# Kernel optimization log

Hardware: AMD Instinct MI355X
Metric: run time of the kernel (lower is better)

The kernel has to match this reference:

```python
import jax, jax.numpy as jnp
import numpy as np

NEG_BIG = -9e15  # matches torch's -9000000000000000.0 mask value
LRELU_ALPHA = 0.2


def setup_inputs() -> dict:
    key = jax.random.key(0)
    ks = jax.random.split(key, 6)
    B, N, Fin, Fout = 2, 4096, 64, 64
    x = jax.random.normal(ks[0], (B, N, Fin), jnp.float32)
    pos = jax.random.normal(ks[1], (B, N, 3), jnp.float32)
    # xavier-ish scaled params
    W = jax.random.normal(ks[2], (Fin, Fout), jnp.float32) * (1.0 / np.sqrt(Fin))
    a = jax.random.normal(ks[3], (2 * Fout, 1), jnp.float32) * (1.0 / np.sqrt(2 * Fout))
    Wp = jax.random.normal(ks[4], (3, Fout), jnp.float32) * (1.0 / np.sqrt(3))
    bp = jnp.zeros((Fout,), jnp.float32)
    return {"x": x, "pos": pos, "W": W, "a": a, "Wp": Wp, "bp": bp, "k": 20}


def reference(x, pos, W, a, Wp, bp, k):
    B, N, _ = x.shape
    Fout = W.shape[1]
    Wh = x @ W  # [B,N,Fout]

    # Dynamic kNN graph (adj=None path): squared-distance ranking == cdist ranking
    sq = jnp.sum(pos * pos, axis=-1)  # [B,N]
    d2 = sq[:, :, None] + sq[:, None, :] - 2.0 * jnp.einsum('bnd,bmd->bnm', pos, pos)
    _, idx = jax.lax.top_k(-d2, k + 1)  # smallest k+1 distances
    idx = idx[:, :, 1:]  # drop self
    adj = jnp.zeros((B, N, N), x.dtype).at[
        jnp.arange(B)[:, None, None], jnp.arange(N)[None, :, None], idx
    ].set(1.0)

    # e[b,i,j] = leakyrelu(a1.Wh_i + a2.Wh_j); decompose instead of O(N^2*2F) concat
    f1 = Wh @ a[:Fout]  # [B,N,1]
    f2 = Wh @ a[Fout:]  # [B,N,1]
    e = f1 + jnp.swapaxes(f2, 1, 2)  # [B,N,N]
    e = jnp.where(e > 0, e, LRELU_ALPHA * e)

    e = jnp.where(adj > 0, e, NEG_BIG)
    attn = jax.nn.softmax(e, axis=2)  # dropout is identity in eval mode

    h = jnp.einsum('bnm,bmf->bnf', attn, Wh) + jax.nn.relu(pos @ Wp + bp)
    return jax.nn.elu(h)  # concat=True path
```

## Files before the change

kernel.cpp:

```cpp
#include <hip/hip_runtime.h>
#include <cfloat>

#define NB 4096
#define FD 64
#define EPT 16
#define QPB 4
#define LRELU_ALPHA 0.2f
#define CCAP 128

__global__ void wa_kernel(const float* __restrict__ W, const float* __restrict__ a,
                          float* __restrict__ wa) {
    const int t = threadIdx.x;
    const float* av = a + ((t >> 6) << 6);
    const int i = t & 63;
    float s = 0.f;
    #pragma unroll
    for (int j = 0; j < FD; ++j) s = fmaf(W[i * FD + j], av[j], s);
    wa[t] = s;
}

__global__ __launch_bounds__(256) void gat_fused(
    const float* __restrict__ x, const float* __restrict__ pos,
    const float* __restrict__ W, const float* __restrict__ wa,
    const float* __restrict__ Wp, const float* __restrict__ bp,
    const int* __restrict__ kptr, float* __restrict__ out)
{
    __shared__ unsigned long long upool[QPB * CCAP];
    __shared__ float4 sq[QPB];
    __shared__ float sT[QPB];
    __shared__ unsigned int cnt[QPB];
    __shared__ int idx21[QPB][64];

    float* tmin = (float*)upool;
    unsigned long long (*cand)[CCAP] = (unsigned long long(*)[CCAP])upool;

    const int tid = threadIdx.x;
    const int lane = tid & 63, wave = tid >> 6;
    const int qbase = blockIdx.x * QPB;
    const int b = qbase >> 12;
    const float* posb = pos + (size_t)b * NB * 3;
    const int k = *kptr;

    if (tid < QPB) {
        const int nq = (qbase + tid) & (NB - 1);
        const float ax = posb[nq * 3 + 0], ay = posb[nq * 3 + 1], az = posb[nq * 3 + 2];
        const float sr = __fadd_rn(__fadd_rn(__fmul_rn(ax, ax), __fmul_rn(ay, ay)),
                                   __fmul_rn(az, az));
        sq[tid] = make_float4(ax, ay, az, sr);
        cnt[tid] = 0;
    }
    __syncthreads();

    const float4 q0 = sq[0], q1 = sq[1], q2 = sq[2], q3 = sq[3];

    const float4* p4 = (const float4*)posb;
    float f0 = FLT_MAX, f1m = FLT_MAX, f2m = FLT_MAX, f3m = FLT_MAX;
    #pragma unroll
    for (int c = 0; c < 4; ++c) {
        const float4 a0 = p4[tid * 12 + c * 3 + 0];
        const float4 a1 = p4[tid * 12 + c * 3 + 1];
        const float4 a2 = p4[tid * 12 + c * 3 + 2];
        const float pxs[4] = {a0.x, a0.w, a1.z, a2.y};
        const float pys[4] = {a0.y, a1.x, a1.w, a2.z};
        const float pzs[4] = {a0.z, a1.y, a2.x, a2.w};
        #pragma unroll
        for (int j = 0; j < 4; ++j) {
            const float px = pxs[j], py = pys[j], pz = pzs[j];
            const float sm = fmaf(pz, pz, fmaf(py, py, px * px));
            float d;
            d = fmaf(-2.f, fmaf(q0.x, px, fmaf(q0.y, py, q0.z * pz)), q0.w + sm);
            f0 = fminf(f0, d);
            d = fmaf(-2.f, fmaf(q1.x, px, fmaf(q1.y, py, q1.z * pz)), q1.w + sm);
            f1m = fminf(f1m, d);
            d = fmaf(-2.f, fmaf(q2.x, px, fmaf(q2.y, py, q2.z * pz)), q2.w + sm);
            f2m = fminf(f2m, d);
            d = fmaf(-2.f, fmaf(q3.x, px, fmaf(q3.y, py, q3.z * pz)), q3.w + sm);
            f3m = fminf(f3m, d);
        }
    }
    tmin[0 * 256 + tid] = f0;  tmin[1 * 256 + tid] = f1m;
    tmin[2 * 256 + tid] = f2m; tmin[3 * 256 + tid] = f3m;
    __syncthreads();

    float v = fminf(fminf(tmin[wave * 256 + lane],       tmin[wave * 256 + 64 + lane]),
                    fminf(tmin[wave * 256 + 128 + lane], tmin[wave * 256 + 192 + lane]));
    #pragma unroll
    for (int kk2 = 2; kk2 <= 64; kk2 <<= 1) {
        #pragma unroll
        for (int j = kk2 >> 1; j > 0; j >>= 1) {
            const float o = __shfl_xor(v, j, 64);
            const bool keepMin = (((lane & j) == 0) == ((lane & kk2) == 0));
            v = keepMin ? fminf(v, o) : fmaxf(v, o);
        }
    }
    const float Tq = __shfl(v, k, 64);
    if (lane == 0) sT[wave] = Tq;
    __syncthreads();

    const float Ts0 = sT[0] + 1e-2f + 1e-3f * fabsf(sT[0]);
    const float Ts1 = sT[1] + 1e-2f + 1e-3f * fabsf(sT[1]);
    const float Ts2 = sT[2] + 1e-2f + 1e-3f * fabsf(sT[2]);
    const float Ts3 = sT[3] + 1e-2f + 1e-3f * fabsf(sT[3]);

    #pragma unroll
    for (int c = 0; c < 4; ++c) {
        const float4 a0 = p4[tid * 12 + c * 3 + 0];
        const float4 a1 = p4[tid * 12 + c * 3 + 1];
        const float4 a2 = p4[tid * 12 + c * 3 + 2];
        const float pxs[4] = {a0.x, a0.w, a1.z, a2.y};
        const float pys[4] = {a0.y, a1.x, a1.w, a2.z};
        const float pzs[4] = {a0.z, a1.y, a2.x, a2.w};
        #pragma unroll
        for (int j = 0; j < 4; ++j) {
            const float px = pxs[j], py = pys[j], pz = pzs[j];
            const float sm = fmaf(pz, pz, fmaf(py, py, px * px));
            const int m = tid * EPT + c * 4 + j;
            #pragma unroll
            for (int q = 0; q < QPB; ++q) {
                const float4 qq = (q == 0) ? q0 : (q == 1) ? q1 : (q == 2) ? q2 : q3;
                const float Tsl = (q == 0) ? Ts0 : (q == 1) ? Ts1 : (q == 2) ? Ts2 : Ts3;
                const float d = fmaf(-2.f, fmaf(qq.x, px, fmaf(qq.y, py, qq.z * pz)),
                                     qq.w + sm);
                if (d <= Tsl) {
                    const float sqm = __fadd_rn(__fadd_rn(__fmul_rn(px, px),
                                                          __fmul_rn(py, py)),
                                                __fmul_rn(pz, pz));
                    const float dot = __fadd_rn(__fadd_rn(__fmul_rn(qq.x, px),
                                                          __fmul_rn(qq.y, py)),
                                                __fmul_rn(qq.z, pz));
                    const float d2 = __fsub_rn(__fadd_rn(qq.w, sqm),
                                               __fmul_rn(2.0f, dot));
                    const unsigned int u = __float_as_uint(d2);
                    const unsigned int kk = u ^ ((unsigned int)((int)u >> 31) | 0x80000000u);
                    const unsigned long long pk =
                        ((unsigned long long)kk << 12) | (unsigned int)m;
                    const unsigned int p = atomicAdd(&cnt[q], 1u);
                    if (p < CCAP) cand[q][p] = pk;
                }
            }
        }
    }
    __syncthreads();

    const int cn0 = (int)cnt[wave];
    const int cn = cn0 < CCAP ? cn0 : CCAP;
    for (int e = lane; e < cn; e += 64) {
        const unsigned long long xv = cand[wave][e];
        int r = 0;
        for (int j = 0; j < cn; ++j) r += (cand[wave][j] < xv);
        if (r <= k) idx21[wave][r] = (int)(xv & 0xFFFu);
    }

    const int row = qbase + wave;
    const int nself = row & (NB - 1);
    const float4 qq = sq[wave];
    const float* xb = x + (((size_t)b << 12) << 6);
    const float wa1v = wa[lane], wa2v = wa[FD + lane];

    float p1 = xb[((size_t)nself << 6) + lane] * wa1v;
    #pragma unroll
    for (int off = 32; off > 0; off >>= 1) p1 += __shfl_xor(p1, off, 64);
    const float f1v = p1;

    float esc = 0.f;
    for (int t = 1; t <= k; ++t) {
        const int nb_ = idx21[wave][t];
        float pm = xb[((size_t)nb_ << 6) + lane] * wa2v;
        #pragma unroll
        for (int off = 32; off > 0; off >>= 1) pm += __shfl_xor(pm, off, 64);
        if (lane == t) esc = pm;
    }
    const bool valid = (lane >= 1 && lane <= k);
    float e = valid ? f1v + esc : -FLT_MAX;
    if (valid) e = e > 0.f ? e : LRELU_ALPHA * e;
    float mx = e;
    #pragma unroll
    for (int off = 32; off > 0; off >>= 1) mx = fmaxf(mx, __shfl_xor(mx, off, 64));
    const float ex = valid ? __expf(e - mx) : 0.f;
    float Z = ex;
    #pragma unroll
    for (int off = 32; off > 0; off >>= 1) Z += __shfl_xor(Z, off, 64);
    const float attn = ex / Z;

    float g = 0.f;
    for (int t = 1; t <= k; ++t) {
        const int nb_ = idx21[wave][t];
        const float xr = xb[((size_t)nb_ << 6) + lane];
        g = fmaf(__shfl(attn, t, 64), xr, g);
    }

    float h = 0.f;
    #pragma unroll 8
    for (int kk = 0; kk < FD; ++kk)
        h = fmaf(__shfl(g, kk, 64), W[kk * FD + lane], h);

    const float pv = fmaf(qq.x, Wp[0 * FD + lane],
                     fmaf(qq.y, Wp[1 * FD + lane],
                     fmaf(qq.z, Wp[2 * FD + lane], bp[lane])));
    h += pv > 0.f ? pv : 0.f;
    out[((size_t)row << 6) + lane] = h > 0.f ? h : expm1f(h);
}

extern "C" void kernel_launch(void* const* d_in, const int* in_sizes, int n_in,
                              void* d_out, int out_size, void* d_ws, size_t ws_size,
                              hipStream_t stream) {
    const float* x   = (const float*)d_in[0];
    const float* pos = (const float*)d_in[1];
    const float* W   = (const float*)d_in[2];
    const float* a   = (const float*)d_in[3];
    const float* Wp  = (const float*)d_in[4];
    const float* bp  = (const float*)d_in[5];
    const int*   kp  = (const int*)d_in[6];
    float* wa  = (float*)d_ws;
    float* out = (float*)d_out;

    wa_kernel<<<1, 128, 0, stream>>>(W, a, wa);
    gat_fused<<<(NB * 2) / QPB, 256, 0, stream>>>(x, pos, W, wa, Wp, bp, kp, out);
}
```

Measured before the change: 111.7 us.

## Precompute Wh and attention logits in prep kernel; defer exact distance to candidates

```diff
diff --git a/kernel.cpp b/kernel.cpp
--- a/kernel.cpp
+++ b/kernel.cpp
@@ -3,36 +3,59 @@
 
 #define NB 4096
 #define FD 64
-#define EPT 16
 #define QPB 4
 #define LRELU_ALPHA 0.2f
-#define CCAP 128
-
-__global__ void wa_kernel(const float* __restrict__ W, const float* __restrict__ a,
-                          float* __restrict__ wa) {
-    const int t = threadIdx.x;
-    const float* av = a + ((t >> 6) << 6);
-    const int i = t & 63;
-    float s = 0.f;
-    #pragma unroll
-    for (int j = 0; j < FD; ++j) s = fmaf(W[i * FD + j], av[j], s);
-    wa[t] = s;
+#define CCAP 96
+
+__global__ __launch_bounds__(256) void prep_kernel(
+    const float* __restrict__ x, const float* __restrict__ W,
+    const float* __restrict__ a,
+    float* __restrict__ Wh, float* __restrict__ f1, float* __restrict__ f2)
+{
+    __shared__ float sW[FD * FD];
+    const int tid = threadIdx.x;
+    #pragma unroll
+    for (int t = 0; t < 16; ++t) sW[tid + t * 256] = W[tid + t * 256];
+    __syncthreads();
+    const int lane = tid & 63, wave = tid >> 6;
+    const float a1v = a[lane], a2v = a[FD + lane];
+    const int rbase = blockIdx.x * 32 + wave * 8;
+    #pragma unroll 2
+    for (int j = 0; j < 8; ++j) {
+        const int row = rbase + j;
+        const float xv = x[((size_t)row << 6) + lane];
+        float acc = 0.f;
+        #pragma unroll
+        for (int i = 0; i < FD; ++i)
+            acc = fmaf(__shfl(xv, i, 64), sW[i * FD + lane], acc);
+        Wh[((size_t)row << 6) + lane] = acc;
+        float r1 = acc * a1v, r2 = acc * a2v;
+        #pragma unroll
+        for (int off = 32; off > 0; off >>= 1) {
+            r1 += __shfl_down(r1, off, 64);
+            r2 += __shfl_down(r2, off, 64);
+        }
+        if (lane == 0) { f1[row] = r1; f2[row] = r2; }
+    }
 }
 
 __global__ __launch_bounds__(256) void gat_fused(
-    const float* __restrict__ x, const float* __restrict__ pos,
-    const float* __restrict__ W, const float* __restrict__ wa,
+    const float* __restrict__ pos, const float* __restrict__ Wh,
+    const float* __restrict__ f1, const float* __restrict__ f2,
     const float* __restrict__ Wp, const float* __restrict__ bp,
     const int* __restrict__ kptr, float* __restrict__ out)
 {
-    __shared__ unsigned long long upool[QPB * CCAP];
+    __shared__ union Pool {
+        float tmin[QPB * 256];
+        struct {
+            unsigned long long pkbuf[QPB][CCAP];
+            int cidx[QPB][CCAP];
+        } s;
+    } pool;
     __shared__ float4 sq[QPB];
     __shared__ float sT[QPB];
     __shared__ unsigned int cnt[QPB];
-    __shared__ int idx21[QPB][64];
-
-    float* tmin = (float*)upool;
-    unsigned long long (*cand)[CCAP] = (unsigned long long(*)[CCAP])upool;
+    __shared__ int idx21[QPB][24];
 
     const int tid = threadIdx.x;
     const int lane = tid & 63, wave = tid >> 6;
@@ -49,6 +72,7 @@
         sq[tid] = make_float4(ax, ay, az, sr);
         cnt[tid] = 0;
     }
+    if (lane < 24) idx21[wave][lane] = (qbase + wave) & (NB - 1);
     __syncthreads();
 
     const float4 q0 = sq[0], q1 = sq[1], q2 = sq[2], q3 = sq[3];
@@ -78,12 +102,14 @@
             f3m = fminf(f3m, d);
         }
     }
-    tmin[0 * 256 + tid] = f0;  tmin[1 * 256 + tid] = f1m;
-    tmin[2 * 256 + tid] = f2m; tmin[3 * 256 + tid] = f3m;
-    __syncthreads();
-
-    float v = fminf(fminf(tmin[wave * 256 + lane],       tmin[wave * 256 + 64 + lane]),
-                    fminf(tmin[wave * 256 + 128 + lane], tmin[wave * 256 + 192 + lane]));
+    pool.tmin[0 * 256 + tid] = f0;  pool.tmin[1 * 256 + tid] = f1m;
+    pool.tmin[2 * 256 + tid] = f2m; pool.tmin[3 * 256 + tid] = f3m;
+    __syncthreads();
+
+    float v = fminf(fminf(pool.tmin[wave * 256 + lane],
+                          pool.tmin[wave * 256 + 64 + lane]),
+                    fminf(pool.tmin[wave * 256 + 128 + lane],
+                          pool.tmin[wave * 256 + 192 + lane]));
     #pragma unroll
     for (int kk2 = 2; kk2 <= 64; kk2 <<= 1) {
         #pragma unroll
@@ -114,65 +140,65 @@
         for (int j = 0; j < 4; ++j) {
             const float px = pxs[j], py = pys[j], pz = pzs[j];
             const float sm = fmaf(pz, pz, fmaf(py, py, px * px));
-            const int m = tid * EPT + c * 4 + j;
-            #pragma unroll
-            for (int q = 0; q < QPB; ++q) {
-                const float4 qq = (q == 0) ? q0 : (q == 1) ? q1 : (q == 2) ? q2 : q3;
-                const float Tsl = (q == 0) ? Ts0 : (q == 1) ? Ts1 : (q == 2) ? Ts2 : Ts3;
-                const float d = fmaf(-2.f, fmaf(qq.x, px, fmaf(qq.y, py, qq.z * pz)),
-                                     qq.w + sm);
-                if (d <= Tsl) {
-                    const float sqm = __fadd_rn(__fadd_rn(__fmul_rn(px, px),
-                                                          __fmul_rn(py, py)),
-                                                __fmul_rn(pz, pz));
-                    const float dot = __fadd_rn(__fadd_rn(__fmul_rn(qq.x, px),
-                                                          __fmul_rn(qq.y, py)),
-                                                __fmul_rn(qq.z, pz));
-                    const float d2 = __fsub_rn(__fadd_rn(qq.w, sqm),
-                                               __fmul_rn(2.0f, dot));
-                    const unsigned int u = __float_as_uint(d2);
-                    const unsigned int kk = u ^ ((unsigned int)((int)u >> 31) | 0x80000000u);
-                    const unsigned long long pk =
-                        ((unsigned long long)kk << 12) | (unsigned int)m;
-                    const unsigned int p = atomicAdd(&cnt[q], 1u);
-                    if (p < CCAP) cand[q][p] = pk;
-                }
-            }
-        }
-    }
-    __syncthreads();
-
+            const int m = tid * 16 + c * 4 + j;
+            float d;
+            d = fmaf(-2.f, fmaf(q0.x, px, fmaf(q0.y, py, q0.z * pz)), q0.w + sm);
+            if (d <= Ts0) {
+                const unsigned int p = atomicAdd(&cnt[0], 1u);
+                if (p < CCAP) pool.s.cidx[0][p] = m;
+            }
+            d = fmaf(-2.f, fmaf(q1.x, px, fmaf(q1.y, py, q1.z * pz)), q1.w + sm);
+            if (d <= Ts1) {
+                const unsigned int p = atomicAdd(&cnt[1], 1u);
+                if (p < CCAP) pool.s.cidx[1][p] = m;
+            }
+            d = fmaf(-2.f, fmaf(q2.x, px, fmaf(q2.y, py, q2.z * pz)), q2.w + sm);
+            if (d <= Ts2) {
+                const unsigned int p = atomicAdd(&cnt[2], 1u);
+                if (p < CCAP) pool.s.cidx[2][p] = m;
+            }
+            d = fmaf(-2.f, fmaf(q3.x, px, fmaf(q3.y, py, q3.z * pz)), q3.w + sm);
+            if (d <= Ts3) {
+                const unsigned int p = atomicAdd(&cnt[3], 1u);
+                if (p < CCAP) pool.s.cidx[3][p] = m;
+            }
+        }
+    }
+    __syncthreads();
+
+    const float4 qq = sq[wave];
     const int cn0 = (int)cnt[wave];
     const int cn = cn0 < CCAP ? cn0 : CCAP;
     for (int e = lane; e < cn; e += 64) {
-        const unsigned long long xv = cand[wave][e];
+        const int m = pool.s.cidx[wave][e];
+        const float px = posb[m * 3 + 0];
+        const float py = posb[m * 3 + 1];
+        const float pz = posb[m * 3 + 2];
+        const float sqm = __fadd_rn(__fadd_rn(__fmul_rn(px, px), __fmul_rn(py, py)),
+                                    __fmul_rn(pz, pz));
+        const float dot = __fadd_rn(__fadd_rn(__fmul_rn(qq.x, px), __fmul_rn(qq.y, py)),
+                                    __fmul_rn(qq.z, pz));
+        const float d2 = __fsub_rn(__fadd_rn(qq.w, sqm), __fmul_rn(2.0f, dot));
+        const unsigned int u = __float_as_uint(d2);
+        const unsigned int kk = u ^ ((unsigned int)((int)u >> 31) | 0x80000000u);
+        pool.s.pkbuf[wave][e] = ((unsigned long long)kk << 12) | (unsigned int)m;
+    }
+    for (int e = lane; e < cn; e += 64) {
+        const unsigned long long xv = pool.s.pkbuf[wave][e];
         int r = 0;
-        for (int j = 0; j < cn; ++j) r += (cand[wave][j] < xv);
+        for (int j = 0; j < cn; ++j) r += (pool.s.pkbuf[wave][j] < xv);
         if (r <= k) idx21[wave][r] = (int)(xv & 0xFFFu);
     }
 
     const int row = qbase + wave;
-    const int nself = row & (NB - 1);
-    const float4 qq = sq[wave];
-    const float* xb = x + (((size_t)b << 12) << 6);
-    const float wa1v = wa[lane], wa2v = wa[FD + lane];
-
-    float p1 = xb[((size_t)nself << 6) + lane] * wa1v;
-    #pragma unroll
-    for (int off = 32; off > 0; off >>= 1) p1 += __shfl_xor(p1, off, 64);
-    const float f1v = p1;
-
-    float esc = 0.f;
-    for (int t = 1; t <= k; ++t) {
-        const int nb_ = idx21[wave][t];
-        float pm = xb[((size_t)nb_ << 6) + lane] * wa2v;
-        #pragma unroll
-        for (int off = 32; off > 0; off >>= 1) pm += __shfl_xor(pm, off, 64);
-        if (lane == t) esc = pm;
-    }
     const bool valid = (lane >= 1 && lane <= k);
-    float e = valid ? f1v + esc : -FLT_MAX;
-    if (valid) e = e > 0.f ? e : LRELU_ALPHA * e;
+    const int nbr = valid ? idx21[wave][lane] : 0;
+    const float f1v = f1[row];
+    float e = -FLT_MAX;
+    if (valid) {
+        e = f1v + f2[(b << 12) + nbr];
+        e = e > 0.f ? e : LRELU_ALPHA * e;
+    }
     float mx = e;
     #pragma unroll
     for (int off = 32; off > 0; off >>= 1) mx = fmaxf(mx, __shfl_xor(mx, off, 64));
@@ -182,17 +208,14 @@
     for (int off = 32; off > 0; off >>= 1) Z += __shfl_xor(Z, off, 64);
     const float attn = ex / Z;
 
-    float g = 0.f;
+    const float* whb = Wh + (((size_t)b << 12) << 6);
+    float h = 0.f;
+    #pragma unroll 4
     for (int t = 1; t <= k; ++t) {
-        const int nb_ = idx21[wave][t];
-        const float xr = xb[((size_t)nb_ << 6) + lane];
-        g = fmaf(__shfl(attn, t, 64), xr, g);
-    }
-
-    float h = 0.f;
-    #pragma unroll 8
-    for (int kk = 0; kk < FD; ++kk)
-        h = fmaf(__shfl(g, kk, 64), W[kk * FD + lane], h);
+        const int nb_ = __shfl(nbr, t, 64);
+        const float s = __shfl(attn, t, 64);
+        h = fmaf(s, whb[((size_t)nb_ << 6) + lane], h);
+    }
 
     const float pv = fmaf(qq.x, Wp[0 * FD + lane],
                      fmaf(qq.y, Wp[1 * FD + lane],
@@ -211,9 +234,13 @@
     const float* Wp  = (const float*)d_in[4];
     const float* bp  = (const float*)d_in[5];
     const int*   kp  = (const int*)d_in[6];
-    float* wa  = (float*)d_ws;
+
+    float* ws = (float*)d_ws;
+    float* Wh = ws;
+    float* f1 = Wh + 524288;
+    float* f2 = f1 + 8192;
     float* out = (float*)d_out;
 
-    wa_kernel<<<1, 128, 0, stream>>>(W, a, wa);
-    gat_fused<<<(NB * 2) / QPB, 256, 0, stream>>>(x, pos, W, wa, Wp, bp, kp, out);
+    prep_kernel<<<256, 256, 0, stream>>>(x, W, a, Wh, f1, f2);
+    gat_fused<<<(NB * 2) / QPB, 256, 0, stream>>>(pos, Wh, f1, f2, Wp, bp, kp, out);
 }
```

Result: slower. 114.4 us (+2.4%).
